# Kernel tuning notes

Hardware: AMD Instinct MI355X
Metric: run time of the kernel (lower is better)

The kernel has to match this reference:

```python
import jax, jax.numpy as jnp
import numpy as np

TEMPERATURE = 0.1
NORM_EPS = 1e-12          # F.normalize default eps
SMALL_VAL = float(np.finfo(np.float32).tiny)  # pytorch-metric-learning small_val(float32)
NEG_INF = float(np.finfo(np.float32).min)     # c_f.neg_inf for masked logsumexp


def setup_inputs() -> dict:
    key = jax.random.key(0)
    k1, k2 = jax.random.split(key)
    N, D = 8192, 128
    emb = jax.random.normal(k1, (N, D), dtype=jnp.float32)
    labels = jax.random.randint(k2, (N,), 0, 1000, dtype=jnp.int64)
    return {"emb": emb, "labels": labels}


def reference(emb, labels):
    N = emb.shape[0]
    # F.normalize(emb, dim=1): x / max(||x||, eps)
    norms = jnp.linalg.norm(emb, axis=1, keepdims=True)
    x = emb / jnp.maximum(norms, NORM_EPS)

    # cosine similarity matrix [N, N], scaled by temperature
    mat = jnp.matmul(x, x.T) / TEMPERATURE

    same = labels[:, None] == labels[None, :]
    diag = jnp.eye(N, dtype=bool)
    pos_mask = same & ~diag          # same label, i != j
    keep_mask = ~diag                # pos + neg (all off-diagonal)

    # numerical stability: subtract detached row max (over full row, incl. diagonal)
    mat_max = jax.lax.stop_gradient(jnp.max(mat, axis=1, keepdims=True))
    mat = mat - mat_max

    # masked logsumexp over off-diagonal entries
    masked = jnp.where(keep_mask, mat, NEG_INF)
    denom = jax.nn.logsumexp(masked, axis=1, keepdims=True)  # [N, 1]

    log_prob = mat - denom
    pos_f = pos_mask.astype(mat.dtype)
    mean_log_prob_pos = jnp.sum(pos_f * log_prob, axis=1) / (
        jnp.sum(pos_f, axis=1) + SMALL_VAL
    )
    losses = -mean_log_prob_pos  # per-element losses
    # SumReducer: sum over elements
    return jnp.sum(losses)
```

## Files before the change

### kernel.cpp

```cpp
#include <hip/hip_runtime.h>
#include <hip/hip_bf16.h>


typedef __bf16 bf16_t;
typedef __bf16 bf16x2 __attribute__((ext_vector_type(2)));
typedef __bf16 bf16x8 __attribute__((ext_vector_type(8)));
typedef float f32x16 __attribute__((ext_vector_type(16)));

#define NN 8192
#define DIM 128
#define MAIN_BLOCKS 2080
#define SMALL_VAL 1.17549435e-38f
#define L2E10 14.4269504089f
#define LN2 0.69314718056f

__device__ inline size_t swz(int row, int lane) {
    int f = lane >> 3, hh = (lane >> 2) & 1, j = (lane & 3) << 1;
    return ((size_t)(row >> 5) * 4096) + f * 512 + hh * 256 + (row & 31) * 8 + j;
}

__global__ __launch_bounds__(256) void norm_csum(const float* __restrict__ emb,
                                                 const int* __restrict__ labels,
                                                 bf16_t* __restrict__ xsw,
                                                 float* __restrict__ cd_arr,
                                                 float* __restrict__ sd_arr,
                                                 float* __restrict__ cm1_arr,
                                                 float* __restrict__ se_acc,
                                                 float* __restrict__ out) {
    __shared__ float cs[DIM];
    __shared__ int rowlist[96];
    __shared__ int nrows;
    int cls = blockIdx.x;
    int wv = threadIdx.x >> 6, lane = threadIdx.x & 63;
    if (threadIdx.x < DIM) cs[threadIdx.x] = 0.f;
    if (threadIdx.x == 0) nrows = 0;
    if (threadIdx.x < 8) se_acc[cls * 8 + threadIdx.x] = 0.f;
    if (cls == 0 && threadIdx.x == 0) *out = 0.f;
    __syncthreads();

    float s0 = 0.f, s1 = 0.f;
    const int4* lab4 = (const int4*)(labels + wv * 2048);
#pragma unroll
    for (int it = 0; it < 8; ++it) {
        int4 l = lab4[it * 64 + lane];
        int base = wv * 2048 + it * 256;
#pragma unroll
        for (int cmp = 0; cmp < 4; ++cmp) {
            int li = (cmp == 0) ? l.x : (cmp == 1) ? l.y : (cmp == 2) ? l.z : l.w;
            unsigned long long m = __ballot(li == cls);
            while (m) {
                int bb = __builtin_ctzll(m);
                m &= m - 1;
                int row = base + 4 * bb + cmp;
                float2 v = ((const float2*)emb)[row * 64 + lane];
                float ss = fmaf(v.x, v.x, v.y * v.y);
#pragma unroll
                for (int mm = 1; mm < 64; mm <<= 1) ss += __shfl_xor(ss, mm, 64);
                float inv = 1.0f / fmaxf(sqrtf(ss), 1e-12f);
                bf16x2 o; o.x = (bf16_t)(v.x * inv); o.y = (bf16_t)(v.y * inv);
                *(bf16x2*)(xsw + swz(row, lane)) = o;
                s0 += (float)o.x; s1 += (float)o.y;
                if (lane == 0) {
                    int idx = atomicAdd(&nrows, 1);
                    if (idx < 96) rowlist[idx] = row;
                }
            }
        }
    }
    atomicAdd(&cs[2 * lane], s0);
    atomicAdd(&cs[2 * lane + 1], s1);
    __syncthreads();
    int n = nrows;
    for (int k = wv; k < n; k += 4) {
        int row = rowlist[k];
        bf16x2 xv = *(const bf16x2*)(xsw + swz(row, lane));
        float x0 = (float)xv.x, x1 = (float)xv.y;
        float cdp = fmaf(x0, cs[2 * lane], x1 * cs[2 * lane + 1]);
        float sdp = fmaf(x0, x0, x1 * x1);
#pragma unroll
        for (int mm = 1; mm < 64; mm <<= 1) {
            cdp += __shfl_xor(cdp, mm, 64);
            sdp += __shfl_xor(sdp, mm, 64);
        }
        if (lane == 0) {
            cd_arr[row] = cdp; sd_arr[row] = sdp; cm1_arr[row] = (float)(n - 1);
        }
    }
}

__global__ __launch_bounds__(256, 4) void supcon_main(const bf16_t* __restrict__ xsw,
                                                      float* __restrict__ se_acc) {
    __shared__ bf16_t bst[4 * 4096];
    __shared__ float cols[128];
    if (threadIdx.x < 128) cols[threadIdx.x] = 0.f;

    int b = blockIdx.x;
    int cq = (int)((sqrtf(8.f * (float)b + 1.f) - 1.f) * 0.5f);
    while ((cq + 1) * (cq + 2) / 2 <= b) ++cq;
    while (cq * (cq + 1) / 2 > b) --cq;
    int g = b - cq * (cq + 1) / 2;

    int wv = threadIdx.x >> 6, lane = threadIdx.x & 63;
    int I = 4 * g + wv;
    int c = lane & 31, h = lane >> 5;
    int laneoff = h * 256 + c * 8;

    const bf16_t* abase = xsw + (size_t)I * 4096 + laneoff;
    bf16x8 a[8];
#pragma unroll
    for (int f = 0; f < 8; ++f) a[f] = *(const bf16x8*)(abase + f * 512);

    {
        const uint4* gsrc = (const uint4*)(xsw + (size_t)cq * 4 * 4096);
        uint4* ldst = (uint4*)bst;
#pragma unroll
        for (int i = 0; i < 8; ++i)
            ldst[i * 256 + threadIdx.x] = gsrc[i * 256 + threadIdx.x];
    }
    __syncthreads();

    float se[16];
#pragma unroll
    for (int r = 0; r < 16; ++r) se[r] = 0.f;
    float colacc[4] = {0.f, 0.f, 0.f, 0.f};

#pragma unroll
    for (int t = 0; t < 4; ++t) {
        const bf16_t* bt = bst + t * 4096 + laneoff;
        bf16x8 bfr[8];
#pragma unroll
        for (int f = 0; f < 8; ++f) bfr[f] = *(const bf16x8*)(bt + f * 512);
        f32x16 acc;
#pragma unroll
        for (int r = 0; r < 16; ++r) acc[r] = 0.f;
#pragma unroll
        for (int f = 0; f < 8; ++f)
            acc = __builtin_amdgcn_mfma_f32_32x32x16_bf16(a[f], bfr[f], acc, 0, 0, 0);
        int ct = cq * 4 + t;
        if (ct >= I) {
            float c0 = 0.f, c1 = 0.f, c2 = 0.f, c3 = 0.f;
#pragma unroll
            for (int r = 0; r < 16; ++r) {
                float e = __builtin_amdgcn_exp2f(fmaf(acc[r], L2E10, -L2E10));
                se[r] += e;
                if ((r & 3) == 0) c0 += e; else if ((r & 3) == 1) c1 += e;
                else if ((r & 3) == 2) c2 += e; else c3 += e;
            }
            if (ct > I) colacc[t] = (c0 + c1) + (c2 + c3);
        }
    }

#pragma unroll
    for (int r = 0; r < 16; ++r) {
        float vv = se[r];
#pragma unroll
        for (int m = 1; m < 32; m <<= 1) vv += __shfl_xor(vv, m, 64);
        se[r] = vv;
    }
    if (c == 0) {
        int rowbase = I * 32 + 4 * h;
#pragma unroll
        for (int r = 0; r < 16; ++r)
            atomicAdd(&se_acc[rowbase + (r & 3) + 8 * (r >> 2)], se[r]);
    }

#pragma unroll
    for (int t = 0; t < 4; ++t) {
        float v = colacc[t] + __shfl_xor(colacc[t], 32, 64);
        if (h == 0) atomicAdd(&cols[t * 32 + c], v);
    }
    __syncthreads();
    if (threadIdx.x < 128)
        atomicAdd(&se_acc[cq * 128 + threadIdx.x], cols[threadIdx.x]);
}

__global__ __launch_bounds__(256) void finalize_kernel(const float* __restrict__ se_acc,
                                                       const float* __restrict__ cd_arr,
                                                       const float* __restrict__ sd_arr,
                                                       const float* __restrict__ cm1_arr,
                                                       float* __restrict__ out) {
    __shared__ float part[4];
    int i = blockIdx.x * 256 + threadIdx.x;
    float sd = sd_arr[i], cd = cd_arr[i], cm1 = cm1_arr[i];
    float diag = __builtin_amdgcn_exp2f(fmaf(sd, L2E10, -L2E10));
    float sev  = fmaxf(se_acc[i] - diag, 1e-30f);
    float lse  = fmaf(__builtin_amdgcn_logf(sev), LN2, 10.f);
    float loss = (cm1 * lse - 10.f * (cd - sd)) / (cm1 + SMALL_VAL);
#pragma unroll
    for (int m = 1; m < 64; m <<= 1) loss += __shfl_xor(loss, m, 64);
    int wv = threadIdx.x >> 6;
    if ((threadIdx.x & 63) == 0) part[wv] = loss;
    __syncthreads();
    if (threadIdx.x == 0) atomicAdd(out, part[0] + part[1] + part[2] + part[3]);
}

extern "C" void kernel_launch(void* const* d_in, const int* in_sizes, int n_in,
                              void* d_out, int out_size, void* d_ws, size_t ws_size,
                              hipStream_t stream) {
    const float* emb  = (const float*)d_in[0];
    const int* labels = (const int*)d_in[1];

    char* ws = (char*)d_ws;
    bf16_t* xsw = (bf16_t*)ws;
    float* se   = (float*)(ws + (size_t)NN * DIM * 2);
    float* cd   = se + NN;
    float* sd   = cd + NN;
    float* cm1  = sd + NN;

    norm_csum<<<1024, 256, 0, stream>>>(emb, labels, xsw, cd, sd, cm1, se, (float*)d_out);
    supcon_main<<<MAIN_BLOCKS, 256, 0, stream>>>(xsw, se);
    finalize_kernel<<<NN / 256, 256, 0, stream>>>(se, cd, sd, cm1, (float*)d_out);
}
```

Baseline: 98.61 us.

## Pipeline LDS fragment loads, use DPP reductions and direct-to-LDS global loads

The main kernel now fills the B tile with global_load_lds instead of staging through registers, and double-buffers its per-tile LDS fragment reads so the next tile loads while the current MFMAs run. It splits the MFMA chain into two independent accumulators to shorten the dependency chain. Row sums are reduced with DPP row operations instead of xor shuffles, and column partial sums go straight to global atomics, which removes the shared cols buffer and its barrier. Occupancy is raised to 5 blocks per CU, which increases register pressure and the number of global atomics issued.

```diff
diff --git a/kernel.cpp b/kernel.cpp
--- a/kernel.cpp
+++ b/kernel.cpp
@@ -17,6 +17,28 @@
 __device__ inline size_t swz(int row, int lane) {
     int f = lane >> 3, hh = (lane >> 2) & 1, j = (lane & 3) << 1;
     return ((size_t)(row >> 5) * 4096) + f * 512 + hh * 256 + (row & 31) * 8 + j;
+}
+
+#define DPPADD(v, ctrl, rmask)                                                         \
+    do {                                                                               \
+        int _t = __builtin_amdgcn_update_dpp(0, __float_as_int((v)), (ctrl), (rmask),  \
+                                             0xf, true);                               \
+        (v) += __int_as_float(_t);                                                     \
+    } while (0)
+
+__device__ inline float half32_sum(float v) {
+    DPPADD(v, 0x111, 0xf);
+    DPPADD(v, 0x112, 0xf);
+    DPPADD(v, 0x114, 0xf);
+    DPPADD(v, 0x118, 0xf);
+    DPPADD(v, 0x142, 0xa);
+    return v;
+}
+
+__device__ inline void gload_lds16(const bf16_t* g, bf16_t* l) {
+    __builtin_amdgcn_global_load_lds(
+        (const __attribute__((address_space(1))) unsigned int*)g,
+        (__attribute__((address_space(3))) unsigned int*)l, 16, 0, 0);
 }
 
 __global__ __launch_bounds__(256) void norm_csum(const float* __restrict__ emb,
@@ -88,11 +110,9 @@
     }
 }
 
-__global__ __launch_bounds__(256, 4) void supcon_main(const bf16_t* __restrict__ xsw,
+__global__ __launch_bounds__(256, 5) void supcon_main(const bf16_t* __restrict__ xsw,
                                                       float* __restrict__ se_acc) {
     __shared__ bf16_t bst[4 * 4096];
-    __shared__ float cols[128];
-    if (threadIdx.x < 128) cols[threadIdx.x] = 0.f;
 
     int b = blockIdx.x;
     int cq = (int)((sqrtf(8.f * (float)b + 1.f) - 1.f) * 0.5f);
@@ -111,67 +131,69 @@
     for (int f = 0; f < 8; ++f) a[f] = *(const bf16x8*)(abase + f * 512);
 
     {
-        const uint4* gsrc = (const uint4*)(xsw + (size_t)cq * 4 * 4096);
-        uint4* ldst = (uint4*)bst;
-#pragma unroll
-        for (int i = 0; i < 8; ++i)
-            ldst[i * 256 + threadIdx.x] = gsrc[i * 256 + threadIdx.x];
+        const bf16_t* gsrc = xsw + (size_t)cq * 4 * 4096;
+#pragma unroll
+        for (int i = 0; i < 8; ++i) {
+            int k = i * 4 + wv;
+            gload_lds16(gsrc + k * 512 + lane * 8, bst + k * 512);
+        }
     }
     __syncthreads();
 
     float se[16];
 #pragma unroll
     for (int r = 0; r < 16; ++r) se[r] = 0.f;
-    float colacc[4] = {0.f, 0.f, 0.f, 0.f};
+
+    bf16x8 cur[8], nxt[8];
+#pragma unroll
+    for (int f = 0; f < 8; ++f) cur[f] = *(const bf16x8*)(bst + laneoff + f * 512);
 
 #pragma unroll
     for (int t = 0; t < 4; ++t) {
-        const bf16_t* bt = bst + t * 4096 + laneoff;
-        bf16x8 bfr[8];
-#pragma unroll
-        for (int f = 0; f < 8; ++f) bfr[f] = *(const bf16x8*)(bt + f * 512);
-        f32x16 acc;
-#pragma unroll
-        for (int r = 0; r < 16; ++r) acc[r] = 0.f;
-#pragma unroll
-        for (int f = 0; f < 8; ++f)
-            acc = __builtin_amdgcn_mfma_f32_32x32x16_bf16(a[f], bfr[f], acc, 0, 0, 0);
+        if (t < 3) {
+            const bf16_t* btn = bst + (t + 1) * 4096 + laneoff;
+#pragma unroll
+            for (int f = 0; f < 8; ++f) nxt[f] = *(const bf16x8*)(btn + f * 512);
+        }
+        f32x16 acc0, acc1;
+#pragma unroll
+        for (int r = 0; r < 16; ++r) { acc0[r] = 0.f; acc1[r] = 0.f; }
+#pragma unroll
+        for (int f = 0; f < 8; f += 2) {
+            acc0 = __builtin_amdgcn_mfma_f32_32x32x16_bf16(a[f], cur[f], acc0, 0, 0, 0);
+            acc1 = __builtin_amdgcn_mfma_f32_32x32x16_bf16(a[f + 1], cur[f + 1], acc1, 0, 0, 0);
+        }
         int ct = cq * 4 + t;
         if (ct >= I) {
             float c0 = 0.f, c1 = 0.f, c2 = 0.f, c3 = 0.f;
 #pragma unroll
             for (int r = 0; r < 16; ++r) {
-                float e = __builtin_amdgcn_exp2f(fmaf(acc[r], L2E10, -L2E10));
+                float s = acc0[r] + acc1[r];
+                float e = __builtin_amdgcn_exp2f(fmaf(s, L2E10, -L2E10));
                 se[r] += e;
                 if ((r & 3) == 0) c0 += e; else if ((r & 3) == 1) c1 += e;
                 else if ((r & 3) == 2) c2 += e; else c3 += e;
             }
-            if (ct > I) colacc[t] = (c0 + c1) + (c2 + c3);
-        }
-    }
-
-#pragma unroll
-    for (int r = 0; r < 16; ++r) {
-        float vv = se[r];
-#pragma unroll
-        for (int m = 1; m < 32; m <<= 1) vv += __shfl_xor(vv, m, 64);
-        se[r] = vv;
-    }
-    if (c == 0) {
+            if (ct > I) {
+                float v = (c0 + c1) + (c2 + c3);
+                v += __shfl_xor(v, 32, 64);
+                if (h == 0) atomicAdd(&se_acc[ct * 32 + c], v);
+            }
+        }
+        if (t < 3) {
+#pragma unroll
+            for (int f = 0; f < 8; ++f) cur[f] = nxt[f];
+        }
+    }
+
+#pragma unroll
+    for (int r = 0; r < 16; ++r) se[r] = half32_sum(se[r]);
+    if (c == 31) {
         int rowbase = I * 32 + 4 * h;
 #pragma unroll
         for (int r = 0; r < 16; ++r)
             atomicAdd(&se_acc[rowbase + (r & 3) + 8 * (r >> 2)], se[r]);
     }
-
-#pragma unroll
-    for (int t = 0; t < 4; ++t) {
-        float v = colacc[t] + __shfl_xor(colacc[t], 32, 64);
-        if (h == 0) atomicAdd(&cols[t * 32 + c], v);
-    }
-    __syncthreads();
-    if (threadIdx.x < 128)
-        atomicAdd(&se_acc[cq * 128 + threadIdx.x], cols[threadIdx.x]);
 }
 
 __global__ __launch_bounds__(256) void finalize_kernel(const float* __restrict__ se_acc,
```

Result: slower. 112.6 us (+14.2%).
